# Kernel tuning notes

Hardware: AMD Instinct MI355X
Metric: run time of the kernel (lower is better)

Reference implementation:

```python
import jax, jax.numpy as jnp
import numpy as np

COMMITMENT_COST = 0.25
EPS = 1e-10


def setup_inputs() -> dict:
    key = jax.random.key(0)
    k1, k2 = jax.random.split(key)
    x = jax.random.normal(k1, (64, 4096, 64), dtype=jnp.float32)          # [B, T, D]
    embedding = jax.random.normal(k2, (512, 64), dtype=jnp.float32)       # [K, D] codebook
    return {"x": x, "embedding": embedding}


def reference(x, embedding):
    B, T, D = x.shape
    K = embedding.shape[0]
    flat = x.reshape(-1, D)                                               # [N, D]
    N = flat.shape[0]

    distances = (jnp.sum(flat * flat, axis=1, keepdims=True)
                 - 2.0 * (flat @ embedding.T)
                 + jnp.sum(embedding * embedding, axis=1))

    idx = jnp.argmin(distances, axis=1)                                   # [N] nearest code
    quantized = embedding[idx].reshape(x.shape)                           # gather lookup

    # commitment loss (EMA variant: only e_latent_loss, codebook frozen w.r.t. loss)
    e_latent_loss = jnp.mean((jax.lax.stop_gradient(quantized) - x) ** 2)
    loss = COMMITMENT_COST * e_latent_loss

    # straight-through estimator
    q_st = x + jax.lax.stop_gradient(quantized - x)

    # perplexity via scatter-add histogram of code usage
    counts = jnp.zeros((K,), dtype=x.dtype).at[idx].add(jnp.ones((), x.dtype))
    avg_probs = counts / jnp.asarray(N, x.dtype)
    perplexity = jnp.exp(-jnp.sum(avg_probs * jnp.log(avg_probs + EPS)))

    return q_st, loss, perplexity
```

## Files before the change

### kernel.cpp

```cpp
#include <hip/hip_runtime.h>
#include <math.h>

#define N_ROWS   262144
#define DIM      64
#define KCODES   512
#define NTHREADS 512
#define NBLOCKS  256
#define TILES    4
#define ESTR     72
#define MARGIN   2e-3f

typedef float f32x4 __attribute__((ext_vector_type(4)));
typedef short s16x8 __attribute__((ext_vector_type(8)));
typedef short s16x4 __attribute__((ext_vector_type(4)));


__device__ __forceinline__ unsigned short f2bf(float f) {
    unsigned u = __float_as_uint(f);
    unsigned r = u + 0x7fffu + ((u >> 16) & 1u);
    return (unsigned short)(r >> 16);
}
__device__ __forceinline__ float bf2f(unsigned short h) {
    return __uint_as_float(((unsigned)h) << 16);
}

__global__ __launch_bounds__(NTHREADS, 2) void vq_main(
    const float* __restrict__ x, const float* __restrict__ emb,
    unsigned short* __restrict__ g_idx, float* __restrict__ g_lossPart,
    unsigned* __restrict__ g_mask, float* __restrict__ out)
{
    __shared__ unsigned short ehs[KCODES * ESTR];
    __shared__ unsigned short els[KCODES * ESTR];
    __shared__ float esq_s[KCODES];
    __shared__ unsigned short idx_sh[8][32];
    __shared__ unsigned short flg_sh[8][32];
    __shared__ float wred[8];

    const int tid  = threadIdx.x;
    const int w    = tid >> 6;
    const int lane = tid & 63;
    const int m    = lane & 15;
    const int q    = lane >> 4;

    if (tid < 32) g_mask[blockIdx.x * 32 + tid] = 0u;

    {
        const float* e = emb + (size_t)tid * DIM;
        float s = 0.f;
        #pragma unroll
        for (int d4 = 0; d4 < DIM; d4 += 4) {
            f32x4 v = *(const f32x4*)&e[d4];
            s += v.x * v.x; s += v.y * v.y; s += v.z * v.z; s += v.w * v.w;
        }
        esq_s[tid] = s;
    }

    #pragma unroll 4
    for (int i = 0; i < 16; ++i) {
        int f = tid + NTHREADS * i;
        int code = f >> 4, d4 = (f & 15) * 4;
        f32x4 v = *(const f32x4*)&emb[(size_t)code * DIM + d4];
        s16x4 hv, lv;
        #pragma unroll
        for (int j = 0; j < 4; ++j) {
            unsigned short h = f2bf(v[j]);
            hv[j] = (short)h;
            lv[j] = (short)f2bf(v[j] - bf2f(h));
        }
        *(s16x4*)&ehs[code * ESTR + d4] = hv;
        *(s16x4*)&els[code * ESTR + d4] = lv;
    }
    __syncthreads();

    float lpart = 0.f;
    const int waveRow0 = blockIdx.x * (NTHREADS / 64 * TILES * 32) + w * (TILES * 32);

    for (int t = 0; t < TILES; ++t) {
        const int T0 = waveRow0 + t * 32;

        f32x4 xv[2][2][2];
        #pragma unroll
        for (int rg = 0; rg < 2; ++rg) {
            const float* px = &x[(size_t)(T0 + rg * 16 + m) * DIM + q * 8];
            xv[rg][0][0] = *(const f32x4*)&px[0];
            xv[rg][0][1] = *(const f32x4*)&px[4];
            xv[rg][1][0] = *(const f32x4*)&px[32];
            xv[rg][1][1] = *(const f32x4*)&px[36];
        }
        s16x8 axh[2][2], axl[2][2];
        #pragma unroll
        for (int rg = 0; rg < 2; ++rg)
            #pragma unroll
            for (int kc = 0; kc < 2; ++kc) {
                s16x8 h, l;
                #pragma unroll
                for (int hf = 0; hf < 2; ++hf)
                    #pragma unroll
                    for (int j = 0; j < 4; ++j) {
                        float v = xv[rg][kc][hf][j];
                        unsigned short hb = f2bf(v);
                        h[hf * 4 + j] = (short)hb;
                        l[hf * 4 + j] = (short)f2bf(v - bf2f(hb));
                    }
                axh[rg][kc] = h; axl[rg][kc] = l;
            }

        float b1[2][4], b2[2][4]; int i1[2][4];
        #pragma unroll
        for (int rg = 0; rg < 2; ++rg)
            #pragma unroll
            for (int r = 0; r < 4; ++r) { b1[rg][r] = 3.4e38f; b2[rg][r] = 3.4e38f; i1[rg][r] = 0; }

        for (int p = 0; p < 4; ++p) {
            f32x4 acc[2][8];
            #pragma unroll
            for (int rg = 0; rg < 2; ++rg)
                #pragma unroll
                for (int cg = 0; cg < 8; ++cg) acc[rg][cg] = (f32x4){0.f, 0.f, 0.f, 0.f};

            #pragma unroll
            for (int kc = 0; kc < 2; ++kc) {
                #pragma unroll
                for (int cg = 0; cg < 8; ++cg) {
                    const int off = (p * 128 + cg * 16 + m) * ESTR + kc * 32 + q * 8;
                    s16x8 bh = *(const s16x8*)&ehs[off];
                    s16x8 bl = *(const s16x8*)&els[off];
                    acc[0][cg] = __builtin_amdgcn_mfma_f32_16x16x32_bf16(axh[0][kc], bh, acc[0][cg], 0, 0, 0);
                    acc[0][cg] = __builtin_amdgcn_mfma_f32_16x16x32_bf16(axl[0][kc], bh, acc[0][cg], 0, 0, 0);
                    acc[0][cg] = __builtin_amdgcn_mfma_f32_16x16x32_bf16(axh[0][kc], bl, acc[0][cg], 0, 0, 0);
                    acc[1][cg] = __builtin_amdgcn_mfma_f32_16x16x32_bf16(axh[1][kc], bh, acc[1][cg], 0, 0, 0);
                    acc[1][cg] = __builtin_amdgcn_mfma_f32_16x16x32_bf16(axl[1][kc], bh, acc[1][cg], 0, 0, 0);
                    acc[1][cg] = __builtin_amdgcn_mfma_f32_16x16x32_bf16(axh[1][kc], bl, acc[1][cg], 0, 0, 0);
                }
            }
            #pragma unroll
            for (int cg = 0; cg < 8; ++cg) {
                int col = p * 128 + cg * 16 + m;
                float e2 = esq_s[col];
                #pragma unroll
                for (int rg = 0; rg < 2; ++rg)
                    #pragma unroll
                    for (int r = 0; r < 4; ++r) {
                        float dist = e2 - 2.f * acc[rg][cg][r];
                        if (dist < b1[rg][r]) { b2[rg][r] = b1[rg][r]; b1[rg][r] = dist; i1[rg][r] = col; }
                        else if (dist < b2[rg][r]) b2[rg][r] = dist;
                    }
            }
        }

        #pragma unroll
        for (int s = 1; s < 16; s <<= 1) {
            #pragma unroll
            for (int rg = 0; rg < 2; ++rg)
                #pragma unroll
                for (int r = 0; r < 4; ++r) {
                    float ob1 = __shfl_xor(b1[rg][r], s);
                    int   oi1 = __shfl_xor(i1[rg][r], s);
                    float ob2 = __shfl_xor(b2[rg][r], s);
                    bool owin = (ob1 < b1[rg][r]) || (ob1 == b1[rg][r] && oi1 < i1[rg][r]);
                    float lb1 = owin ? b1[rg][r] : ob1;
                    b2[rg][r] = fminf(fminf(b2[rg][r], ob2), lb1);
                    if (owin) { b1[rg][r] = ob1; i1[rg][r] = oi1; }
                }
        }
        if (m == 0) {
            #pragma unroll
            for (int rg = 0; rg < 2; ++rg)
                #pragma unroll
                for (int r = 0; r < 4; ++r) {
                    int rl = rg * 16 + q * 4 + r;
                    int fl = (b2[rg][r] - b1[rg][r] < MARGIN) ? 1 : 0;
                    idx_sh[w][rl] = (unsigned short)i1[rg][r];
                    flg_sh[w][rl] = (unsigned short)fl;
                    if (fl) {
                        int grow = T0 + rl;
                        atomicOr(&g_mask[grow >> 5], 1u << (grow & 31));
                    }
                }
        }
        if (lane < 32) g_idx[T0 + lane] = idx_sh[w][lane];

        #pragma unroll
        for (int rg = 0; rg < 2; ++rg) {
            int rl = rg * 16 + m;
            int ki = idx_sh[w][rl];
            int fl = flg_sh[w][rl];
            if (!fl) {
                const float* er = &emb[(size_t)ki * DIM + q * 8];
                float* po = &out[(size_t)(T0 + rl) * DIM + q * 8];
                #pragma unroll
                for (int kc = 0; kc < 2; ++kc)
                    #pragma unroll
                    for (int hf = 0; hf < 2; ++hf) {
                        f32x4 ev = *(const f32x4*)&er[kc * 32 + hf * 4];
                        f32x4 xvv = xv[rg][kc][hf];
                        f32x4 fd, o;
                        #pragma unroll
                        for (int j = 0; j < 4; ++j) {
                            fd[j] = ev[j] - xvv[j];
                            o[j]  = xvv[j] + fd[j];
                            lpart += fd[j] * fd[j];
                        }
                        *(f32x4*)&po[kc * 32 + hf * 4] = o;
                    }
            }
        }
    }

    #pragma unroll
    for (int s = 32; s > 0; s >>= 1) lpart += __shfl_down(lpart, s);
    if (lane == 0) wred[w] = lpart;
    __syncthreads();
    if (tid == 0) {
        float s = 0.f;
        #pragma unroll
        for (int i = 0; i < 8; ++i) s += wred[i];
        g_lossPart[blockIdx.x] = s;
    }
}

__global__ __launch_bounds__(256) void vq_post(
    const float* __restrict__ x, const float* __restrict__ emb,
    unsigned short* __restrict__ g_idx, const unsigned* __restrict__ g_mask,
    float* __restrict__ out, int* __restrict__ counts2d,
    float* __restrict__ lossPost)
{
    __shared__ int h[KCODES];
    __shared__ float lred[4];
    const int b    = blockIdx.x;
    const int tid  = threadIdx.x;
    const int wv   = tid >> 6;
    const int lane = tid & 63;

    float lp = 0.f;
    for (int wi = 0; wi < 32; ++wi) {
        unsigned mw = g_mask[b * 128 + wv * 32 + wi];
        while (mw) {
            int bit = __ffs(mw) - 1;
            mw &= mw - 1;
            int row = b * 4096 + wv * 1024 + wi * 32 + bit;
            const float* xr = &x[(size_t)row * DIM];
            float best = 3.4e38f; int bidx = 0;
            #pragma unroll
            for (int j = 0; j < 8; ++j) {
                int c = lane * 8 + j;
                const float* er = &emb[(size_t)c * DIM];
                float es = 0.f;
                #pragma unroll
                for (int d4 = 0; d4 < DIM; d4 += 4) {
                    f32x4 v = *(const f32x4*)&er[d4];
                    es += v.x * v.x; es += v.y * v.y; es += v.z * v.z; es += v.w * v.w;
                }
                float dot = 0.f;
                #pragma unroll
                for (int d = 0; d < DIM; ++d) dot = fmaf(xr[d], er[d], dot);
                float dist = es - 2.f * dot;
                if (dist < best) { best = dist; bidx = c; }
            }
            #pragma unroll
            for (int s = 1; s < 64; s <<= 1) {
                float ob = __shfl_xor(best, s);
                int   oi = __shfl_xor(bidx, s);
                if (ob < best || (ob == best && oi < bidx)) { best = ob; bidx = oi; }
            }
            float xvv = xr[lane];
            float ev  = emb[(size_t)bidx * DIM + lane];
            float f   = ev - xvv;
            out[(size_t)row * DIM + lane] = xvv + f;
            lp += f * f;
            if (lane == 0) g_idx[row] = (unsigned short)bidx;
        }
    }
    #pragma unroll
    for (int s = 32; s > 0; s >>= 1) lp += __shfl_down(lp, s);
    if (lane == 0) lred[wv] = lp;
    __threadfence();
    __syncthreads();

    h[tid] = 0; h[tid + 256] = 0;
    __syncthreads();
    const unsigned short* p = g_idx + (size_t)b * 4096;
    #pragma unroll
    for (int i = 0; i < 16; ++i)
        atomicAdd(&h[p[tid + 256 * i]], 1);
    __syncthreads();
    counts2d[b * KCODES + tid]       = h[tid];
    counts2d[b * KCODES + tid + 256] = h[tid + 256];
    if (tid == 0) lossPost[b] = lred[0] + lred[1] + lred[2] + lred[3];
}

__global__ __launch_bounds__(512) void vq_final(const int* __restrict__ counts2d,
                                                const float* __restrict__ lossPart,
                                                const float* __restrict__ lossPost,
                                                float* __restrict__ out) {
    __shared__ float redp[8], redl[8];
    int k = threadIdx.x;
    int c = 0;
    for (int b = 0; b < 64; ++b) c += counts2d[b * KCODES + k];
    float p = (float)c * (1.f / 262144.f);
    float t = p * logf(p + 1e-10f);
    float l = 0.f;
    if (k < 256) l = lossPart[k];
    if (k < 64)  l += lossPost[k];
    #pragma unroll
    for (int off = 32; off > 0; off >>= 1) {
        t += __shfl_down(t, off);
        l += __shfl_down(l, off);
    }
    if ((k & 63) == 0) { redp[k >> 6] = t; redl[k >> 6] = l; }
    __syncthreads();
    if (k == 0) {
        float s = 0.f, ls = 0.f;
        #pragma unroll
        for (int i = 0; i < 8; ++i) { s += redp[i]; ls += redl[i]; }
        out[16777216] = ls * (0.25f / 16777216.f);
        out[16777217] = expf(-s);
    }
}

extern "C" void kernel_launch(void* const* d_in, const int* in_sizes, int n_in,
                              void* d_out, int out_size, void* d_ws, size_t ws_size,
                              hipStream_t stream) {
    const float* x   = (const float*)d_in[0];
    const float* emb = (const float*)d_in[1];
    float* out = (float*)d_out;

    char* ws = (char*)d_ws;
    unsigned*       mask     = (unsigned*)(ws + 0);
    unsigned short* gidx     = (unsigned short*)(ws + 32768);
    float*          lossPart = (float*)(ws + 557056);
    float*          lossPost = (float*)(ws + 558080);
    int*            counts2d = (int*)(ws + 558336);

    vq_main<<<NBLOCKS, NTHREADS, 0, stream>>>(x, emb, gidx, lossPart, mask, out);
    vq_post<<<64, 256, 0, stream>>>(x, emb, gidx, mask, out, counts2d, lossPost);
    vq_final<<<1, 512, 0, stream>>>(counts2d, lossPart, lossPost, out);
}
```

Before: 266.4 us.

## Fuse ambiguous-row fallback and histogram into main kernel with packed argmin keys

```diff
diff --git a/kernel.cpp b/kernel.cpp
--- a/kernel.cpp
+++ b/kernel.cpp
@@ -8,7 +8,8 @@
 #define NBLOCKS  256
 #define TILES    4
 #define ESTR     72
-#define MARGIN   2e-3f
+#define BIAS     256.0f
+#define T5       16384u
 
 typedef float f32x4 __attribute__((ext_vector_type(4)));
 typedef short s16x8 __attribute__((ext_vector_type(8)));
@@ -23,15 +24,19 @@
 __device__ __forceinline__ float bf2f(unsigned short h) {
     return __uint_as_float(((unsigned)h) << 16);
 }
+__device__ __forceinline__ unsigned umin32(unsigned a, unsigned b) { return a < b ? a : b; }
+__device__ __forceinline__ unsigned umax32(unsigned a, unsigned b) { return a > b ? a : b; }
 
 __global__ __launch_bounds__(NTHREADS, 2) void vq_main(
     const float* __restrict__ x, const float* __restrict__ emb,
-    unsigned short* __restrict__ g_idx, float* __restrict__ g_lossPart,
-    unsigned* __restrict__ g_mask, float* __restrict__ out)
+    int* __restrict__ counts2d, float* __restrict__ g_lossPart,
+    float* __restrict__ out)
 {
     __shared__ unsigned short ehs[KCODES * ESTR];
     __shared__ unsigned short els[KCODES * ESTR];
     __shared__ float esq_s[KCODES];
+    __shared__ float e2b_s[KCODES];
+    __shared__ int   h_sh[KCODES];
     __shared__ unsigned short idx_sh[8][32];
     __shared__ unsigned short flg_sh[8][32];
     __shared__ float wred[8];
@@ -42,7 +47,7 @@
     const int m    = lane & 15;
     const int q    = lane >> 4;
 
-    if (tid < 32) g_mask[blockIdx.x * 32 + tid] = 0u;
+    h_sh[tid] = 0;
 
     {
         const float* e = emb + (size_t)tid * DIM;
@@ -53,6 +58,7 @@
             s += v.x * v.x; s += v.y * v.y; s += v.z * v.z; s += v.w * v.w;
         }
         esq_s[tid] = s;
+        e2b_s[tid] = s + BIAS;
     }
 
     #pragma unroll 4
@@ -72,8 +78,15 @@
     }
     __syncthreads();
 
+    float e2b_reg[32];
+    #pragma unroll
+    for (int p = 0; p < 4; ++p)
+        #pragma unroll
+        for (int cg = 0; cg < 8; ++cg)
+            e2b_reg[p * 8 + cg] = e2b_s[p * 128 + cg * 16 + m];
+
     float lpart = 0.f;
-    const int waveRow0 = blockIdx.x * (NTHREADS / 64 * TILES * 32) + w * (TILES * 32);
+    const int waveRow0 = blockIdx.x * 1024 + w * (TILES * 32);
 
     for (int t = 0; t < TILES; ++t) {
         const int T0 = waveRow0 + t * 32;
@@ -105,11 +118,11 @@
                 axh[rg][kc] = h; axl[rg][kc] = l;
             }
 
-        float b1[2][4], b2[2][4]; int i1[2][4];
+        unsigned m1[2][4], m2[2][4];
         #pragma unroll
         for (int rg = 0; rg < 2; ++rg)
             #pragma unroll
-            for (int r = 0; r < 4; ++r) { b1[rg][r] = 3.4e38f; b2[rg][r] = 3.4e38f; i1[rg][r] = 0; }
+            for (int r = 0; r < 4; ++r) { m1[rg][r] = 0xFFFFFFFFu; m2[rg][r] = 0xFFFFFFFFu; }
 
         for (int p = 0; p < 4; ++p) {
             f32x4 acc[2][8];
@@ -135,75 +148,102 @@
             }
             #pragma unroll
             for (int cg = 0; cg < 8; ++cg) {
-                int col = p * 128 + cg * 16 + m;
-                float e2 = esq_s[col];
+                const unsigned pcg = (unsigned)(p * 8 + cg);
+                const float e2b = e2b_reg[p * 8 + cg];
                 #pragma unroll
                 for (int rg = 0; rg < 2; ++rg)
                     #pragma unroll
                     for (int r = 0; r < 4; ++r) {
-                        float dist = e2 - 2.f * acc[rg][cg][r];
-                        if (dist < b1[rg][r]) { b2[rg][r] = b1[rg][r]; b1[rg][r] = dist; i1[rg][r] = col; }
-                        else if (dist < b2[rg][r]) b2[rg][r] = dist;
+                        float db = fmaf(-2.f, acc[rg][cg][r], e2b);
+                        unsigned u = (__float_as_uint(db) & 0xFFFFFFE0u) | pcg;
+                        unsigned a1 = m1[rg][r];
+                        unsigned mx = umax32(a1, u);
+                        m1[rg][r] = umin32(a1, u);
+                        m2[rg][r] = umin32(m2[rg][r], mx);
                     }
             }
         }
 
+        unsigned om[2][4];
+        #pragma unroll
+        for (int rg = 0; rg < 2; ++rg)
+            #pragma unroll
+            for (int r = 0; r < 4; ++r) om[rg][r] = m1[rg][r];
         #pragma unroll
         for (int s = 1; s < 16; s <<= 1) {
             #pragma unroll
             for (int rg = 0; rg < 2; ++rg)
                 #pragma unroll
                 for (int r = 0; r < 4; ++r) {
-                    float ob1 = __shfl_xor(b1[rg][r], s);
-                    int   oi1 = __shfl_xor(i1[rg][r], s);
-                    float ob2 = __shfl_xor(b2[rg][r], s);
-                    bool owin = (ob1 < b1[rg][r]) || (ob1 == b1[rg][r] && oi1 < i1[rg][r]);
-                    float lb1 = owin ? b1[rg][r] : ob1;
-                    b2[rg][r] = fminf(fminf(b2[rg][r], ob2), lb1);
-                    if (owin) { b1[rg][r] = ob1; i1[rg][r] = oi1; }
-                }
-        }
-        if (m == 0) {
-            #pragma unroll
-            for (int rg = 0; rg < 2; ++rg)
-                #pragma unroll
-                for (int r = 0; r < 4; ++r) {
-                    int rl = rg * 16 + q * 4 + r;
-                    int fl = (b2[rg][r] - b1[rg][r] < MARGIN) ? 1 : 0;
-                    idx_sh[w][rl] = (unsigned short)i1[rg][r];
-                    flg_sh[w][rl] = (unsigned short)fl;
-                    if (fl) {
-                        int grow = T0 + rl;
-                        atomicOr(&g_mask[grow >> 5], 1u << (grow & 31));
-                    }
-                }
-        }
-        if (lane < 32) g_idx[T0 + lane] = idx_sh[w][lane];
+                    unsigned o1 = (unsigned)__shfl_xor((int)m1[rg][r], s);
+                    unsigned o2 = (unsigned)__shfl_xor((int)m2[rg][r], s);
+                    unsigned mx = umax32(m1[rg][r], o1);
+                    m1[rg][r] = umin32(m1[rg][r], o1);
+                    m2[rg][r] = umin32(umin32(m2[rg][r], o2), mx);
+                }
+        }
+        #pragma unroll
+        for (int rg = 0; rg < 2; ++rg)
+            #pragma unroll
+            for (int r = 0; r < 4; ++r) {
+                unsigned g1 = m1[rg][r], g2 = m2[rg][r];
+                int rl = rg * 16 + q * 4 + r;
+                if (om[rg][r] == g1) {
+                    int pcg = (int)(g1 & 31u);
+                    int col = (pcg >> 3) * 128 + (pcg & 7) * 16 + m;
+                    idx_sh[w][rl] = (unsigned short)col;
+                }
+                if (m == 0) flg_sh[w][rl] = (unsigned short)((g2 - g1 < T5) ? 1 : 0);
+            }
+
+        for (int row = 0; row < 32; ++row) {
+            if (flg_sh[w][row]) {
+                int grow = T0 + row;
+                const float* xr = &x[(size_t)grow * DIM];
+                float best = 3.4e38f; int bidx = 0;
+                #pragma unroll
+                for (int j = 0; j < 8; ++j) {
+                    int c = lane * 8 + j;
+                    const float* er = &emb[(size_t)c * DIM];
+                    float dot = 0.f;
+                    #pragma unroll
+                    for (int d = 0; d < DIM; ++d) dot = fmaf(xr[d], er[d], dot);
+                    float dist = esq_s[c] - 2.f * dot;
+                    if (dist < best) { best = dist; bidx = c; }
+                }
+                #pragma unroll
+                for (int s = 1; s < 64; s <<= 1) {
+                    float ob = __shfl_xor(best, s);
+                    int   oi = __shfl_xor(bidx, s);
+                    if (ob < best || (ob == best && oi < bidx)) { best = ob; bidx = oi; }
+                }
+                if (lane == 0) idx_sh[w][row] = (unsigned short)bidx;
+            }
+        }
+
+        if (lane < 32) atomicAdd(&h_sh[idx_sh[w][lane]], 1);
 
         #pragma unroll
         for (int rg = 0; rg < 2; ++rg) {
             int rl = rg * 16 + m;
             int ki = idx_sh[w][rl];
-            int fl = flg_sh[w][rl];
-            if (!fl) {
-                const float* er = &emb[(size_t)ki * DIM + q * 8];
-                float* po = &out[(size_t)(T0 + rl) * DIM + q * 8];
-                #pragma unroll
-                for (int kc = 0; kc < 2; ++kc)
+            const float* er = &emb[(size_t)ki * DIM + q * 8];
+            float* po = &out[(size_t)(T0 + rl) * DIM + q * 8];
+            #pragma unroll
+            for (int kc = 0; kc < 2; ++kc)
+                #pragma unroll
+                for (int hf = 0; hf < 2; ++hf) {
+                    f32x4 ev = *(const f32x4*)&er[kc * 32 + hf * 4];
+                    f32x4 xvv = xv[rg][kc][hf];
+                    f32x4 fd, o;
                     #pragma unroll
-                    for (int hf = 0; hf < 2; ++hf) {
-                        f32x4 ev = *(const f32x4*)&er[kc * 32 + hf * 4];
-                        f32x4 xvv = xv[rg][kc][hf];
-                        f32x4 fd, o;
-                        #pragma unroll
-                        for (int j = 0; j < 4; ++j) {
-                            fd[j] = ev[j] - xvv[j];
-                            o[j]  = xvv[j] + fd[j];
-                            lpart += fd[j] * fd[j];
-                        }
-                        *(f32x4*)&po[kc * 32 + hf * 4] = o;
+                    for (int j = 0; j < 4; ++j) {
+                        fd[j] = ev[j] - xvv[j];
+                        o[j]  = xvv[j] + fd[j];
+                        lpart += fd[j] * fd[j];
                     }
-            }
+                    *(f32x4*)&po[kc * 32 + hf * 4] = o;
+                }
         }
     }
 
@@ -211,6 +251,7 @@
     for (int s = 32; s > 0; s >>= 1) lpart += __shfl_down(lpart, s);
     if (lane == 0) wred[w] = lpart;
     __syncthreads();
+    counts2d[blockIdx.x * KCODES + tid] = h_sh[tid];
     if (tid == 0) {
         float s = 0.f;
         #pragma unroll
@@ -219,89 +260,16 @@
     }
 }
 
-__global__ __launch_bounds__(256) void vq_post(
-    const float* __restrict__ x, const float* __restrict__ emb,
-    unsigned short* __restrict__ g_idx, const unsigned* __restrict__ g_mask,
-    float* __restrict__ out, int* __restrict__ counts2d,
-    float* __restrict__ lossPost)
-{
-    __shared__ int h[KCODES];
-    __shared__ float lred[4];
-    const int b    = blockIdx.x;
-    const int tid  = threadIdx.x;
-    const int wv   = tid >> 6;
-    const int lane = tid & 63;
-
-    float lp = 0.f;
-    for (int wi = 0; wi < 32; ++wi) {
-        unsigned mw = g_mask[b * 128 + wv * 32 + wi];
-        while (mw) {
-            int bit = __ffs(mw) - 1;
-            mw &= mw - 1;
-            int row = b * 4096 + wv * 1024 + wi * 32 + bit;
-            const float* xr = &x[(size_t)row * DIM];
-            float best = 3.4e38f; int bidx = 0;
-            #pragma unroll
-            for (int j = 0; j < 8; ++j) {
-                int c = lane * 8 + j;
-                const float* er = &emb[(size_t)c * DIM];
-                float es = 0.f;
-                #pragma unroll
-                for (int d4 = 0; d4 < DIM; d4 += 4) {
-                    f32x4 v = *(const f32x4*)&er[d4];
-                    es += v.x * v.x; es += v.y * v.y; es += v.z * v.z; es += v.w * v.w;
-                }
-                float dot = 0.f;
-                #pragma unroll
-                for (int d = 0; d < DIM; ++d) dot = fmaf(xr[d], er[d], dot);
-                float dist = es - 2.f * dot;
-                if (dist < best) { best = dist; bidx = c; }
-            }
-            #pragma unroll
-            for (int s = 1; s < 64; s <<= 1) {
-                float ob = __shfl_xor(best, s);
-                int   oi = __shfl_xor(bidx, s);
-                if (ob < best || (ob == best && oi < bidx)) { best = ob; bidx = oi; }
-            }
-            float xvv = xr[lane];
-            float ev  = emb[(size_t)bidx * DIM + lane];
-            float f   = ev - xvv;
-            out[(size_t)row * DIM + lane] = xvv + f;
-            lp += f * f;
-            if (lane == 0) g_idx[row] = (unsigned short)bidx;
-        }
-    }
-    #pragma unroll
-    for (int s = 32; s > 0; s >>= 1) lp += __shfl_down(lp, s);
-    if (lane == 0) lred[wv] = lp;
-    __threadfence();
-    __syncthreads();
-
-    h[tid] = 0; h[tid + 256] = 0;
-    __syncthreads();
-    const unsigned short* p = g_idx + (size_t)b * 4096;
-    #pragma unroll
-    for (int i = 0; i < 16; ++i)
-        atomicAdd(&h[p[tid + 256 * i]], 1);
-    __syncthreads();
-    counts2d[b * KCODES + tid]       = h[tid];
-    counts2d[b * KCODES + tid + 256] = h[tid + 256];
-    if (tid == 0) lossPost[b] = lred[0] + lred[1] + lred[2] + lred[3];
-}
-
-__global__ __launch_bounds__(512) void vq_final(const int* __restrict__ counts2d,
-                                                const float* __restrict__ lossPart,
-                                                const float* __restrict__ lossPost,
-                                                float* __restrict__ out) {
+__global__ __launch_bounds__(512) void vq_fin(const int* __restrict__ counts2d,
+                                              const float* __restrict__ lossPart,
+                                              float* __restrict__ out) {
     __shared__ float redp[8], redl[8];
     int k = threadIdx.x;
     int c = 0;
-    for (int b = 0; b < 64; ++b) c += counts2d[b * KCODES + k];
+    for (int b = 0; b < NBLOCKS; ++b) c += counts2d[b * KCODES + k];
     float p = (float)c * (1.f / 262144.f);
     float t = p * logf(p + 1e-10f);
-    float l = 0.f;
-    if (k < 256) l = lossPart[k];
-    if (k < 64)  l += lossPost[k];
+    float l = (k < 256) ? lossPart[k] : 0.f;
     #pragma unroll
     for (int off = 32; off > 0; off >>= 1) {
         t += __shfl_down(t, off);
@@ -326,13 +294,9 @@
     float* out = (float*)d_out;
 
     char* ws = (char*)d_ws;
-    unsigned*       mask     = (unsigned*)(ws + 0);
-    unsigned short* gidx     = (unsigned short*)(ws + 32768);
-    float*          lossPart = (float*)(ws + 557056);
-    float*          lossPost = (float*)(ws + 558080);
-    int*            counts2d = (int*)(ws + 558336);
-
-    vq_main<<<NBLOCKS, NTHREADS, 0, stream>>>(x, emb, gidx, lossPart, mask, out);
-    vq_post<<<64, 256, 0, stream>>>(x, emb, gidx, mask, out, counts2d, lossPost);
-    vq_final<<<1, 512, 0, stream>>>(counts2d, lossPart, lossPost, out);
-}
+    int*   counts2d = (int*)(ws + 0);
+    float* lossPart = (float*)(ws + 524288);
+
+    vq_main<<<NBLOCKS, NTHREADS, 0, stream>>>(x, emb, counts2d, lossPart, out);
+    vq_fin<<<1, 512, 0, stream>>>(counts2d, lossPart, out);
+}
```

Measured after the change: 611.7 us. +129.6%, slower.
